# Kernel tuning notes

Hardware: AMD Instinct MI355X
Metric: run time of the kernel (lower is better)

The kernel has to match this reference:

```python
import jax, jax.numpy as jnp
import numpy as np

NH = 6
D = 78  # dim_k = dim_v, dk = dv = 13 per head
SCALE = 1.0 / np.sqrt(D // NH).astype(np.float32)


def _split(t):
    # (B, n, D) -> (B, H, n, dk)
    B, n, d = t.shape
    return t.reshape(B, n, NH, d // NH).transpose(0, 2, 1, 3)


def _merge(t):
    # (B, H, n, dk) -> (B, n, D)
    B, h, n, d = t.shape
    return t.transpose(0, 2, 1, 3).reshape(B, n, h * d)


def _cross_attn(x, y, Wq, Wk, Wv):
    # MultiHeadCrossSelfAttention / MultiHeadSelfAttention math (dropout=identity in eval;
    # attn_mask is expanded but never applied in the original forward).
    q = _split(x @ Wq)
    k = _split(y @ Wk)
    v = _split(y @ Wv)
    dist = jax.nn.softmax(jnp.einsum('bhqd,bhkd->bhqk', q, k) * SCALE, axis=-1)
    return _merge(jnp.einsum('bhqk,bhkd->bhqd', dist, v))


def _contrastive_attn(x, y, Wq, Wk, Wv):
    # MultiHeadContrastiveSelfAttention: softmax -> (1 - p) -> softmax -> matmul, residual q add.
    q = _split(x @ Wq)
    k = _split(y @ Wk)
    v = _split(y @ Wv)
    dist = jax.nn.softmax(jnp.einsum('bhqd,bhkd->bhqk', q, k) * SCALE, axis=-1)
    dist = jax.nn.softmax(1.0 - dist, axis=-1)
    return _merge(q + jnp.einsum('bhqk,bhkd->bhqd', dist, v))


def setup_inputs() -> dict:
    key = jax.random.key(0)
    ks = jax.random.split(key, 20)
    B, nT, nV, nA = 8, 1024, 1024, 1024
    inp = {
        'x': jax.random.normal(ks[0], (B, nT, D), jnp.float32),
        'y': jax.random.normal(ks[1], (B, nV, D), jnp.float32),
        'z': jax.random.normal(ks[2], (B, nA, D), jnp.float32),
        'mask_tv': jnp.zeros((B, nT, nV), jnp.bool_),
        'mask_ta': jnp.zeros((B, nT, nA), jnp.bool_),
    }
    names = ['Wq_tv', 'Wk_tv', 'Wv_tv', 'Wq_ta', 'Wk_ta', 'Wv_ta',
             'Wq_ctv', 'Wk_ctv', 'Wv_ctv', 'Wq_cta', 'Wk_cta', 'Wv_cta',
             'Wq_s', 'Wk_s', 'Wv_s']
    for i, nm in enumerate(names):
        inp[nm] = jax.random.normal(ks[3 + i], (D, D), jnp.float32) * 0.05
    return inp


def reference(x, y, z, mask_tv, mask_ta,
              Wq_tv, Wk_tv, Wv_tv, Wq_ta, Wk_ta, Wv_ta,
              Wq_ctv, Wk_ctv, Wv_ctv, Wq_cta, Wk_cta, Wv_cta,
              Wq_s, Wk_s, Wv_s):
    # masks are dead args in the original module (expanded but never applied)
    att_tv = _cross_attn(x, y, Wq_tv, Wk_tv, Wv_tv)          # MHSCA_TV
    att_ta = _cross_attn(x, z, Wq_ta, Wk_ta, Wv_ta)          # MHSCA_TA
    c_tv = _contrastive_attn(x, y, Wq_ctv, Wk_ctv, Wv_ctv)   # MHSCTA_TV
    c_ta = _contrastive_attn(x, z, Wq_cta, Wk_cta, Wv_cta)   # MHSCTA_TA
    # fuse three pooled modality tokens through the length-3 MHSA
    tokens = jnp.stack([x.mean(axis=1),
                        (att_tv + c_tv).mean(axis=1),
                        (att_ta + c_ta).mean(axis=1)], axis=1)  # (B, 3, D)
    fused = _cross_attn(tokens, tokens, Wq_s, Wk_s, Wv_s)       # MHSA
    # (B, 4*1024 + 3, D)
    return jnp.concatenate([att_tv, c_tv, att_ta, c_ta, fused], axis=1)
```

## Files before the change

### kernel.cpp

```cpp
#include <hip/hip_runtime.h>
#include <hip/hip_bf16.h>

#define BB 8
#define NN 1024
#define DM 78
#define NH 6
#define DK 13
#define NROW 4099
#define QSCL 0.40013158f
#define SCALE 0.27735009811261457f
#define INV1023 0.000977517106549365f

using bf16 = __hip_bfloat16;
typedef __attribute__((ext_vector_type(8))) short short8;
typedef __attribute__((ext_vector_type(4))) float f32x4;

#define MATSZ ((size_t)48 * 1024 * 16)

struct PW { const float* w[12]; };

__device__ __forceinline__ unsigned pkbf2(float a, float b) {
    __hip_bfloat162 t = __float22bfloat162_rn(make_float2(a, b));
    return *(unsigned*)&t;
}

__global__ void zero_kernel(float* __restrict__ p, int n) {
    for (int i = threadIdx.x; i < n; i += 256) p[i] = 0.f;
}

__global__ __launch_bounds__(320) void proj_kernel(const float* __restrict__ x,
                                                   const float* __restrict__ y,
                                                   const float* __restrict__ z,
                                                   PW p,
                                                   unsigned* __restrict__ Qbf,
                                                   unsigned* __restrict__ Kbf,
                                                   unsigned* __restrict__ Vt,
                                                   float* __restrict__ Qf32,
                                                   float* __restrict__ sv,
                                                   float* __restrict__ tok) {
    __shared__ float AT[78 * 68];
    __shared__ float WL[78 * 80];
    int bid = blockIdx.x;
    int mat = bid >> 7;
    int rb = bid & 127;
    const float* src = (mat < 4) ? x : (((mat - 4) & 1) ? z : y);
    int tid = threadIdx.x;
    const float* sp = src + (size_t)rb * 64 * DM;
    for (int i = tid; i < 64 * DM; i += 320) {
        int r = i / DM, e = i - r * DM;
        AT[e * 68 + r] = sp[i];
    }
    const float* W = p.w[mat];
    for (int i = tid; i < DM * DM; i += 320) {
        int e = i / DM, c = i - e * DM;
        WL[e * 80 + c] = W[i];
    }
    __syncthreads();
    int rowg = tid / 20, colg = tid % 20;
    float acc[4][4] = {{0.f}};
    for (int e = 0; e < DM; ++e) {
        float4 a = *(const float4*)&AT[e * 68 + rowg * 4];
        float4 w = *(const float4*)&WL[e * 80 + colg * 4];
        acc[0][0] = fmaf(a.x, w.x, acc[0][0]); acc[0][1] = fmaf(a.x, w.y, acc[0][1]);
        acc[0][2] = fmaf(a.x, w.z, acc[0][2]); acc[0][3] = fmaf(a.x, w.w, acc[0][3]);
        acc[1][0] = fmaf(a.y, w.x, acc[1][0]); acc[1][1] = fmaf(a.y, w.y, acc[1][1]);
        acc[1][2] = fmaf(a.y, w.z, acc[1][2]); acc[1][3] = fmaf(a.y, w.w, acc[1][3]);
        acc[2][0] = fmaf(a.z, w.x, acc[2][0]); acc[2][1] = fmaf(a.z, w.y, acc[2][1]);
        acc[2][2] = fmaf(a.z, w.z, acc[2][2]); acc[2][3] = fmaf(a.z, w.w, acc[2][3]);
        acc[3][0] = fmaf(a.w, w.x, acc[3][0]); acc[3][1] = fmaf(a.w, w.y, acc[3][1]);
        acc[3][2] = fmaf(a.w, w.z, acc[3][2]); acc[3][3] = fmaf(a.w, w.w, acc[3][3]);
    }
    __syncthreads();
    float* CT = WL;
#pragma unroll
    for (int j = 0; j < 4; ++j)
#pragma unroll
        for (int k = 0; k < 4; ++k) {
            int c = colg * 4 + k;
            if (c < DM) CT[(rowg * 4 + j) * 81 + c] = acc[j][k];
        }
    __syncthreads();
    int bb = rb >> 4;
    int i0 = (rb & 15) * 64;
    if (mat < 8) {
        unsigned* dst = (mat < 4) ? Qbf : Kbf;
        int m4 = (mat < 4) ? mat : mat - 4;
        float scl = (mat < 4) ? QSCL : 1.0f;
        for (int t2 = tid; t2 < NH * 64 * 8; t2 += 320) {
            int hh = t2 >> 9;
            int rem = t2 & 511;
            int r = rem >> 3, cp = rem & 7;
            int c0 = cp * 2, c1 = cp * 2 + 1;
            float a = (c0 < DK) ? CT[r * 81 + hh * DK + c0] * scl : 0.f;
            float bv = (c1 < DK) ? CT[r * 81 + hh * DK + c1] * scl : 0.f;
            dst[(((size_t)m4 * 48 + bb * NH + hh) * 1024 + i0 + r) * 8 + cp] = pkbf2(a, bv);
        }
        if (mat >= 2) {
            for (int t2 = tid; t2 < 64 * DM; t2 += 320) {
                int r = t2 / DM, c = t2 - r * DM;
                int hh = c / DK, dd = c - hh * DK;
                Qf32[((size_t)(mat - 2) * 48 + bb * NH + hh) * 1024 * DK +
                     (size_t)(i0 + r) * DK + dd] = CT[r * 81 + c];
            }
        }
    } else {
        for (int t2 = tid; t2 < NH * 16 * 32; t2 += 320) {
            int hh = t2 >> 9;
            int rem = t2 & 511;
            int dd = rem >> 5, cp = rem & 31;
            float a, bv;
            if (dd < DK) {
                a = CT[(cp * 2) * 81 + hh * DK + dd];
                bv = CT[(cp * 2 + 1) * 81 + hh * DK + dd];
            } else if (dd == 13) { a = 1.f; bv = 1.f; }
            else { a = 0.f; bv = 0.f; }
            Vt[(((size_t)(mat - 8) * 48 + bb * NH + hh) * 16 + dd) * 512 +
               (i0 >> 1) + cp] = pkbf2(a, bv);
        }
        if (mat >= 10 && tid < DM) {
            int hh = tid / DK, dd = tid - hh * DK;
            float s = 0.f;
            for (int r = 0; r < 64; ++r) s += CT[r * 81 + tid];
            atomicAdd(&sv[((size_t)(mat - 10) * 48 + bb * NH + hh) * DK + dd], s);
        }
    }
    if (mat == 0 && tid < DM) {
        float s = 0.f;
        for (int r = 0; r < 64; ++r) s += AT[tid * 68 + r];
        atomicAdd(&tok[bb * DM + tid], s);
    }
}

__global__ __launch_bounds__(256) void att_kernel(const bf16* __restrict__ Qbf,
                                                  const bf16* __restrict__ Kbf,
                                                  const bf16* __restrict__ Vt,
                                                  const float* __restrict__ Qf32,
                                                  const float* __restrict__ sv,
                                                  float* __restrict__ tok,
                                                  float* __restrict__ out) {
    __shared__ short PL[4 * 640];
    int bid = blockIdx.x;
    int qt = bid & 15;
    int rest = bid >> 4;
    int h = rest % NH; rest /= NH;
    int b = rest & 7;
    int g = rest >> 3;
    int tid = threadIdx.x, wave = tid >> 6, lane = tid & 63;
    int quad = lane >> 4, lq = lane & 15;
    size_t mb = (size_t)g * 48 + b * NH + h;
    int q0 = qt * 64 + wave * 16;

    short8 zero8 = {0, 0, 0, 0, 0, 0, 0, 0};
    short8 qf = zero8;
    if (quad < 2)
        qf = *(const short8*)((const short*)Qbf + (mb * 1024 + q0 + lq) * 16 + quad * 8);
    const short* Kp = (const short*)Kbf + mb * 1024 * 16;
    const short* Vp = (const short*)Vt + mb * 16 * 1024 + (size_t)lq * 1024;
    short* myP = &PL[wave * 640];
    f32x4 O = {0.f, 0.f, 0.f, 0.f};
    const f32x4 zz = {0.f, 0.f, 0.f, 0.f};

    for (int kt = 0; kt < 32; ++kt) {
        int key0 = kt * 32;
        short8 kf0 = zero8, kf1 = zero8;
        if (quad < 2) {
            kf0 = *(const short8*)(Kp + (key0 + lq) * 16 + quad * 8);
            kf1 = *(const short8*)(Kp + (key0 + 16 + lq) * 16 + quad * 8);
        }
        f32x4 S0 = __builtin_amdgcn_mfma_f32_16x16x32_bf16(kf0, qf, zz, 0, 0, 0);
        f32x4 S1 = __builtin_amdgcn_mfma_f32_16x16x32_bf16(kf1, qf, zz, 0, 0, 0);
        uint2 w0, w1;
        w0.x = pkbf2(exp2f(S0[0]), exp2f(S0[1]));
        w0.y = pkbf2(exp2f(S0[2]), exp2f(S0[3]));
        w1.x = pkbf2(exp2f(S1[0]), exp2f(S1[1]));
        w1.y = pkbf2(exp2f(S1[2]), exp2f(S1[3]));
        *(uint2*)(myP + lq * 40 + quad * 4) = w0;
        *(uint2*)(myP + lq * 40 + 16 + quad * 4) = w1;
        asm volatile("s_waitcnt lgkmcnt(0)" ::: "memory");
        short8 pf = *(const short8*)(myP + lq * 40 + quad * 8);
        short8 vf = *(const short8*)(Vp + key0 + quad * 8);
        O = __builtin_amdgcn_mfma_f32_16x16x32_bf16(pf, vf, O, 0, 0, 0);
    }

    size_t rowbase = (g == 0) ? 0 : (g == 1 ? 2 * NN : (g == 2 ? NN : 3 * NN));
    float l[4];
#pragma unroll
    for (int r = 0; r < 4; ++r)
        l[r] = __shfl(O[r], (lane & 48) | 13, 64);
    float svv = 0.f;
    if (g >= 2 && lq < DK)
        svv = sv[((size_t)(g - 2) * 48 + b * NH + h) * DK + lq];
    float vsum = 0.f;
#pragma unroll
    for (int r = 0; r < 4; ++r) {
        int m = q0 + quad * 4 + r;
        float A = O[r] / l[r];
        float val;
        if (g < 2) {
            val = A;
        } else {
            float qres = (lq < DK)
                ? Qf32[((size_t)(g - 2) * 48 + b * NH + h) * 1024 * DK +
                       (size_t)m * DK + lq] : 0.f;
            val = qres + (svv - A) * INV1023;
        }
        if (lq < DK) {
            out[((size_t)b * NROW + rowbase + m) * DM + h * DK + lq] = val;
            vsum += val;
        }
    }
    vsum += __shfl_xor(vsum, 16);
    vsum += __shfl_xor(vsum, 32);
    if (quad == 0 && lq < DK) {
        int tki = (g & 1) ? 2 : 1;
        atomicAdd(&tok[(size_t)tki * (8 * DM) + b * DM + h * DK + lq], vsum);
    }
}

__global__ __launch_bounds__(256) void fused_kernel(const float* __restrict__ tok,
                                                    const float* __restrict__ Wq,
                                                    const float* __restrict__ Wk,
                                                    const float* __restrict__ Wv,
                                                    float* __restrict__ out) {
    __shared__ float T[3 * DM], Qs[3 * DM], Ks[3 * DM], Vs[3 * DM], P[NH * 9];
    int b = blockIdx.x, tid = threadIdx.x;
    if (tid < 234) {
        int t = tid / DM, d = tid - t * DM;
        T[tid] = tok[(size_t)t * (8 * DM) + b * DM + d] * (1.f / NN);
    }
    __syncthreads();
    for (int idx = tid; idx < 702; idx += 256) {
        int mat = idx / 234;
        int rem = idx - mat * 234;
        int t = rem / DM, d = rem - t * DM;
        const float* W = (mat == 0) ? Wq : (mat == 1 ? Wk : Wv);
        float a = 0.f;
        for (int e = 0; e < DM; ++e) a = fmaf(T[t * DM + e], W[(size_t)e * DM + d], a);
        float* dst = (mat == 0) ? Qs : (mat == 1 ? Ks : Vs);
        dst[t * DM + d] = a;
    }
    __syncthreads();
    if (tid < NH * 3) {
        int h = tid / 3, t = tid % 3;
        float s[3];
        for (int k = 0; k < 3; ++k) {
            float a = 0.f;
            for (int d2 = 0; d2 < DK; ++d2)
                a += Qs[t * DM + h * DK + d2] * Ks[k * DM + h * DK + d2];
            s[k] = a * SCALE;
        }
        float mm = fmaxf(s[0], fmaxf(s[1], s[2]));
        float e0 = __expf(s[0] - mm), e1 = __expf(s[1] - mm), e2 = __expf(s[2] - mm);
        float inv = 1.f / (e0 + e1 + e2);
        P[(h * 3 + t) * 3 + 0] = e0 * inv;
        P[(h * 3 + t) * 3 + 1] = e1 * inv;
        P[(h * 3 + t) * 3 + 2] = e2 * inv;
    }
    __syncthreads();
    if (tid < 234) {
        int t = tid / DM, d = tid - t * DM, h = d / DK;
        float a = 0.f;
        for (int k = 0; k < 3; ++k) a += P[(h * 3 + t) * 3 + k] * Vs[k * DM + d];
        out[((size_t)b * NROW + 4 * NN + t) * DM + d] = a;
    }
}

extern "C" void kernel_launch(void* const* d_in, const int* in_sizes, int n_in,
                              void* d_out, int out_size, void* d_ws, size_t ws_size,
                              hipStream_t stream) {
    const float* bigs[3] = {nullptr, nullptr, nullptr};
    const float* w[15];
    int nb = 0, nw = 0;
    for (int i = 0; i < n_in; ++i) {
        if (in_sizes[i] == BB * NN * DM && nb < 3) bigs[nb++] = (const float*)d_in[i];
        else if (in_sizes[i] == DM * DM && nw < 15) w[nw++] = (const float*)d_in[i];
    }
    if (nb < 3 || nw < 15) {
        bigs[0] = (const float*)d_in[0]; bigs[1] = (const float*)d_in[1];
        bigs[2] = (const float*)d_in[2];
        int base = (n_in >= 20) ? 5 : 3;
        for (int i = 0; i < 15; ++i) w[i] = (const float*)d_in[base + i];
    }
    const float* x = bigs[0];
    const float* y = bigs[1];
    const float* z = bigs[2];
    float* out = (float*)d_out;

    bf16* Qbf = (bf16*)d_ws;
    bf16* Kbf = Qbf + 4 * MATSZ;
    bf16* Vt  = Kbf + 4 * MATSZ;
    float* Qf32 = (float*)(Vt + 4 * MATSZ);
    float* sv = Qf32 + (size_t)2 * 48 * 1024 * DK;
    float* tok = sv + 2 * 48 * DK;

    PW pp;
    const float* wsel[12] = {w[0], w[3], w[6], w[9],
                             w[1], w[4], w[7], w[10],
                             w[2], w[5], w[8], w[11]};
    for (int i = 0; i < 12; ++i) pp.w[i] = wsel[i];

    zero_kernel<<<1, 256, 0, stream>>>(sv, 2 * 48 * DK + 3 * 8 * DM);
    proj_kernel<<<1536, 320, 0, stream>>>(x, y, z, pp, (unsigned*)Qbf, (unsigned*)Kbf,
                                          (unsigned*)Vt, Qf32, sv, tok);
    att_kernel<<<4 * BB * NH * 16, 256, 0, stream>>>(Qbf, Kbf, Vt, Qf32, sv, tok, out);
    fused_kernel<<<BB, 256, 0, stream>>>(tok, w[12], w[13], w[14], out);
}
```

Measured before the change: 257.1 us.

## Process two query tiles per wave and prefetch next K/V tile in attention

Each attention wave now computes two 16-row query tiles (offset by 512) that share every K and V fragment load, halving the grid. The K/V fragments for the next key block are loaded before the current block's exp/LDS work, overlapping global latency with compute. The cost is more registers and LDS per block, fewer blocks, and a harmless out-of-range prefetch on the final iteration.

```diff
diff --git a/kernel.cpp b/kernel.cpp
--- a/kernel.cpp
+++ b/kernel.cpp
@@ -138,10 +138,10 @@
                                                   const float* __restrict__ sv,
                                                   float* __restrict__ tok,
                                                   float* __restrict__ out) {
-    __shared__ short PL[4 * 640];
+    __shared__ short PL[4 * 1280];
     int bid = blockIdx.x;
-    int qt = bid & 15;
-    int rest = bid >> 4;
+    int qt = bid & 7;
+    int rest = bid >> 3;
     int h = rest % NH; rest /= NH;
     int b = rest & 7;
     int g = rest >> 3;
@@ -149,26 +149,41 @@
     int quad = lane >> 4, lq = lane & 15;
     size_t mb = (size_t)g * 48 + b * NH + h;
     int q0 = qt * 64 + wave * 16;
+    int q1 = q0 + 512;
 
     short8 zero8 = {0, 0, 0, 0, 0, 0, 0, 0};
-    short8 qf = zero8;
-    if (quad < 2)
-        qf = *(const short8*)((const short*)Qbf + (mb * 1024 + q0 + lq) * 16 + quad * 8);
+    short8 qfA = zero8, qfB = zero8;
+    if (quad < 2) {
+        qfA = *(const short8*)((const short*)Qbf + (mb * 1024 + q0 + lq) * 16 + quad * 8);
+        qfB = *(const short8*)((const short*)Qbf + (mb * 1024 + q1 + lq) * 16 + quad * 8);
+    }
     const short* Kp = (const short*)Kbf + mb * 1024 * 16;
     const short* Vp = (const short*)Vt + mb * 16 * 1024 + (size_t)lq * 1024;
-    short* myP = &PL[wave * 640];
-    f32x4 O = {0.f, 0.f, 0.f, 0.f};
+    short* myP = &PL[wave * 1280];
+    f32x4 OA = {0.f, 0.f, 0.f, 0.f};
+    f32x4 OB = {0.f, 0.f, 0.f, 0.f};
     const f32x4 zz = {0.f, 0.f, 0.f, 0.f};
 
+    short8 kf0 = zero8, kf1 = zero8, vf;
+    if (quad < 2) {
+        kf0 = *(const short8*)(Kp + lq * 16 + quad * 8);
+        kf1 = *(const short8*)(Kp + (16 + lq) * 16 + quad * 8);
+    }
+    vf = *(const short8*)(Vp + quad * 8);
+
     for (int kt = 0; kt < 32; ++kt) {
-        int key0 = kt * 32;
-        short8 kf0 = zero8, kf1 = zero8;
+        int nkey = (kt + 1) * 32;
+        f32x4 S0 = __builtin_amdgcn_mfma_f32_16x16x32_bf16(kf0, qfA, zz, 0, 0, 0);
+        f32x4 S1 = __builtin_amdgcn_mfma_f32_16x16x32_bf16(kf1, qfA, zz, 0, 0, 0);
+        f32x4 S2 = __builtin_amdgcn_mfma_f32_16x16x32_bf16(kf0, qfB, zz, 0, 0, 0);
+        f32x4 S3 = __builtin_amdgcn_mfma_f32_16x16x32_bf16(kf1, qfB, zz, 0, 0, 0);
+        short8 kf0n = zero8, kf1n = zero8, vfn;
         if (quad < 2) {
-            kf0 = *(const short8*)(Kp + (key0 + lq) * 16 + quad * 8);
-            kf1 = *(const short8*)(Kp + (key0 + 16 + lq) * 16 + quad * 8);
-        }
-        f32x4 S0 = __builtin_amdgcn_mfma_f32_16x16x32_bf16(kf0, qf, zz, 0, 0, 0);
-        f32x4 S1 = __builtin_amdgcn_mfma_f32_16x16x32_bf16(kf1, qf, zz, 0, 0, 0);
+            kf0n = *(const short8*)(Kp + (nkey + lq) * 16 + quad * 8);
+            kf1n = *(const short8*)(Kp + (nkey + 16 + lq) * 16 + quad * 8);
+        }
+        vfn = *(const short8*)(Vp + nkey + quad * 8);
+
         uint2 w0, w1;
         w0.x = pkbf2(exp2f(S0[0]), exp2f(S0[1]));
         w0.y = pkbf2(exp2f(S0[2]), exp2f(S0[3]));
@@ -176,37 +191,52 @@
         w1.y = pkbf2(exp2f(S1[2]), exp2f(S1[3]));
         *(uint2*)(myP + lq * 40 + quad * 4) = w0;
         *(uint2*)(myP + lq * 40 + 16 + quad * 4) = w1;
+        w0.x = pkbf2(exp2f(S2[0]), exp2f(S2[1]));
+        w0.y = pkbf2(exp2f(S2[2]), exp2f(S2[3]));
+        w1.x = pkbf2(exp2f(S3[0]), exp2f(S3[1]));
+        w1.y = pkbf2(exp2f(S3[2]), exp2f(S3[3]));
+        *(uint2*)(myP + 640 + lq * 40 + quad * 4) = w0;
+        *(uint2*)(myP + 640 + lq * 40 + 16 + quad * 4) = w1;
         asm volatile("s_waitcnt lgkmcnt(0)" ::: "memory");
-        short8 pf = *(const short8*)(myP + lq * 40 + quad * 8);
-        short8 vf = *(const short8*)(Vp + key0 + quad * 8);
-        O = __builtin_amdgcn_mfma_f32_16x16x32_bf16(pf, vf, O, 0, 0, 0);
+        short8 pfA = *(const short8*)(myP + lq * 40 + quad * 8);
+        short8 pfB = *(const short8*)(myP + 640 + lq * 40 + quad * 8);
+        OA = __builtin_amdgcn_mfma_f32_16x16x32_bf16(pfA, vf, OA, 0, 0, 0);
+        OB = __builtin_amdgcn_mfma_f32_16x16x32_bf16(pfB, vf, OB, 0, 0, 0);
+        kf0 = kf0n; kf1 = kf1n; vf = vfn;
     }
 
     size_t rowbase = (g == 0) ? 0 : (g == 1 ? 2 * NN : (g == 2 ? NN : 3 * NN));
-    float l[4];
+    float lA[4], lB[4];
 #pragma unroll
-    for (int r = 0; r < 4; ++r)
-        l[r] = __shfl(O[r], (lane & 48) | 13, 64);
+    for (int r = 0; r < 4; ++r) {
+        lA[r] = __shfl(OA[r], (lane & 48) | 13, 64);
+        lB[r] = __shfl(OB[r], (lane & 48) | 13, 64);
+    }
     float svv = 0.f;
-    if (g >= 2 && lq < DK)
-        svv = sv[((size_t)(g - 2) * 48 + b * NH + h) * DK + lq];
+    const float* qf32p = nullptr;
+    if (g >= 2) {
+        if (lq < DK) svv = sv[((size_t)(g - 2) * 48 + b * NH + h) * DK + lq];
+        qf32p = Qf32 + ((size_t)(g - 2) * 48 + b * NH + h) * 1024 * DK + lq;
+    }
     float vsum = 0.f;
 #pragma unroll
     for (int r = 0; r < 4; ++r) {
-        int m = q0 + quad * 4 + r;
-        float A = O[r] / l[r];
-        float val;
-        if (g < 2) {
-            val = A;
-        } else {
-            float qres = (lq < DK)
-                ? Qf32[((size_t)(g - 2) * 48 + b * NH + h) * 1024 * DK +
-                       (size_t)m * DK + lq] : 0.f;
-            val = qres + (svv - A) * INV1023;
+        int mA = q0 + quad * 4 + r;
+        int mB = q1 + quad * 4 + r;
+        float A0 = OA[r] / lA[r];
+        float A1 = OB[r] / lB[r];
+        float v0, v1;
+        if (g < 2) { v0 = A0; v1 = A1; }
+        else {
+            float qr0 = (lq < DK) ? qf32p[(size_t)mA * DK] : 0.f;
+            float qr1 = (lq < DK) ? qf32p[(size_t)mB * DK] : 0.f;
+            v0 = qr0 + (svv - A0) * INV1023;
+            v1 = qr1 + (svv - A1) * INV1023;
         }
         if (lq < DK) {
-            out[((size_t)b * NROW + rowbase + m) * DM + h * DK + lq] = val;
-            vsum += val;
+            out[((size_t)b * NROW + rowbase + mA) * DM + h * DK + lq] = v0;
+            out[((size_t)b * NROW + rowbase + mB) * DM + h * DK + lq] = v1;
+            vsum += v0 + v1;
         }
     }
     vsum += __shfl_xor(vsum, 16);
@@ -302,6 +332,6 @@
     zero_kernel<<<1, 256, 0, stream>>>(sv, 2 * 48 * DK + 3 * 8 * DM);
     proj_kernel<<<1536, 320, 0, stream>>>(x, y, z, pp, (unsigned*)Qbf, (unsigned*)Kbf,
                                           (unsigned*)Vt, Qf32, sv, tok);
-    att_kernel<<<4 * BB * NH * 16, 256, 0, stream>>>(Qbf, Kbf, Vt, Qf32, sv, tok, out);
+    att_kernel<<<4 * BB * NH * 8, 256, 0, stream>>>(Qbf, Kbf, Vt, Qf32, sv, tok, out);
     fused_kernel<<<BB, 256, 0, stream>>>(tok, w[12], w[13], w[14], out);
 }
```

Result: faster. 243.6 us (-5.3%).
